# Kernel tuning notes

Measured on AMD Instinct MI355X. Metric: run time of the kernel, lower is better.

The kernel has to match this reference:

```python
import jax, jax.numpy as jnp
import numpy as np

KA = 2  # kernel_att == stride

def _unfold2(t):
    # torch nn.Unfold(kernel=2, stride=2, pad=0): [B,C,H,W] -> [B, C, 4, L], L=(H/2)*(W/2)
    B, C, H, W = t.shape
    t = t.reshape(B, C, H // KA, KA, W // KA, KA).transpose(0, 1, 3, 5, 2, 4)
    return t.reshape(B, C, KA * KA, (H // KA) * (W // KA))

def _fold2(t, H, W):
    # inverse of _unfold2 (non-overlapping): [B, C, 4, L] -> [B, C, H, W]
    B, C, _, L = t.shape
    t = t.reshape(B, C, KA, KA, H // KA, W // KA).transpose(0, 1, 4, 2, 5, 3)
    return t.reshape(B, C, H, W)

def setup_inputs() -> dict:
    key = jax.random.key(0)
    ks = jax.random.split(key, 5)
    b, c, m, h, w = 4, 16, 8, 64, 64
    O = 64
    return {
        "x": jax.random.normal(ks[0], (b, c, m, h, w), jnp.float32),
        "w_q": jax.random.normal(ks[1], (O, m), jnp.float32) * 0.1,
        "w_k": jax.random.normal(ks[2], (O, m), jnp.float32) * 0.1,
        "w_v": jax.random.normal(ks[3], (O, m), jnp.float32) * 0.1,
        "w_p": jax.random.normal(ks[4], (2,), jnp.float32) * 0.1,
    }

def reference(x, w_q, w_k, w_v, w_p):
    b, c, m, h, w = x.shape
    O = w_q.shape[0]
    # res = AdaptiveAvgPool3d((1, dim, dim)) with h==w==dim -> mean over m only
    res = x.mean(axis=2, keepdims=True)            # [b, c, 1, h, w]
    xf = x.reshape(b * c, m, h, w)
    # 1x1 convs (bias-free) are channel matmuls
    q = jnp.einsum('om,bmhw->bohw', w_q, xf)       # [b*c, O, h, w]
    k = jnp.einsum('om,bmhw->bohw', w_k, xf)
    v = jnp.einsum('om,bmhw->bohw', w_v, xf)
    # relative position map pe = conv_p(position(h, w)) -> [1,1,h,w]
    loc_w = jnp.linspace(-1.0, 1.0, w)[None, :]    # varies along W
    loc_h = jnp.linspace(-1.0, 1.0, h)[:, None]    # varies along H
    pe = (w_p[0] * loc_w + w_p[1] * loc_h)[None, None]  # [1,1,h,w]
    q5 = q.reshape(b, c, O, h, w).transpose(0, 2, 1, 3, 4)  # permuted: [b, O, c, h, w]
    k5 = k.reshape(b, c, O, h, w) + pe             # pe broadcast over trailing (h,w)
    v5 = v.reshape(b, c, O, h, w)
    scaling = float(h) ** (-0.5)
    B = b * O
    q_att = (q5 * scaling).reshape(B, c, h, w)
    # NB: torch code views the UNpermuted [b,c,O,h,w] buffer as [b*O, c, h, w] (raw reinterpretation)
    k_att = k5.reshape(B, c, h, w)
    v_att = v5.reshape(B, c, h, w)
    uq = _unfold2(q_att)                           # [B, c, 4, L]
    uk = _unfold2(k_att) + _unfold2(pe)            # unfold_rpe broadcast: [B, c, 4, L]
    uv = _unfold2(v_att)
    # att[B,i,j,l] = sum_p q[B,i,p,l] * k[B,j,p,l]
    att = jnp.einsum('bipl,bjpl->bijl', uq, uk)    # [B, c, c, L]
    att = jax.nn.softmax(att, axis=2)
    out = jnp.einsum('bijl,bjpl->bipl', att, uv)   # [B, c, 4, L]
    out = _fold2(out, h, w)                        # [B, c, h, w]
    out = out.reshape(b, O, c, h, w).transpose(0, 2, 1, 3, 4)  # [b, c, O, h, w]
    return out + res
```

## Files before the change

kernel.cpp:

```cpp
#include <hip/hip_runtime.h>

typedef float v2f __attribute__((ext_vector_type(2)));


__global__ __launch_bounds__(256, 4) void adapt_attn(
    const float* __restrict__ x,  const float* __restrict__ wq,
    const float* __restrict__ wk, const float* __restrict__ wv,
    const float* __restrict__ wp, float* __restrict__ out)
{
    __shared__ __align__(16) float s_wk[128];
    __shared__ __align__(16) float s_wv[128];
    __shared__ v2f    s_xk[2][8][2][16];
    __shared__ float4 s_uk[2][16][16];
    __shared__ float4 s_uv[2][16][16];

    const int tid = threadIdx.x;
    const int bid = blockIdx.x;
    const int tg = bid & 31;
    const int o  = (bid >> 5) & 63;
    const int bb = bid >> 11;
    const int r = o & 3, qch = o >> 2;

    const v2f* __restrict__ x2 = (const v2f*)x;

    v2f s1v[2];
    #pragma unroll
    for (int it = 0; it < 2; it++) {
        const int idx = it * 256 + tid;
        const int p = idx & 15, row = (idx >> 4) & 1, m = (idx >> 5) & 7, t = idx >> 8;
        const int tile = tg * 2 + t;
        const int y0 = (tile >> 1) << 1, ww0 = (tile & 1) << 4;
        s1v[it] = x2[((bb * 16 + qch) * 8 + m) * 2048 + (y0 + row) * 32 + ww0 + p];
    }

    float wkv_k = 0.f, wkv_v = 0.f;
    if (tid < 128) {
        wkv_k = wk[(r << 7) + tid];
        wkv_v = wv[(r << 7) + tid];
    }

    const int p3 = tid & 15, ig = (tid >> 4) & 7, t3 = tid >> 7;
    const int tile3 = tg * 2 + t3;
    const int y03 = (tile3 >> 1) << 1, ww03 = (tile3 & 1) << 4;
    const int sp = y03 * 32 + ww03 + p3;

    v2f qa0[8], qb0[8], qa1[8], qb1[8];
    {
        const int bq0 = (bb * 16 + ig * 2) * 16384 + sp;
        const int bq1 = bq0 + 16384;
        #pragma unroll
        for (int m = 0; m < 8; m++) {
            qa0[m] = x2[bq0 + m * 2048];
            qb0[m] = x2[bq0 + m * 2048 + 32];
            qa1[m] = x2[bq1 + m * 2048];
            qb1[m] = x2[bq1 + m * 2048 + 32];
        }
    }

    #pragma unroll
    for (int it = 0; it < 2; it++) {
        const int idx = it * 256 + tid;
        const int p = idx & 15, row = (idx >> 4) & 1, m = (idx >> 5) & 7, t = idx >> 8;
        s_xk[t][m][row][p] = s1v[it];
    }
    if (tid < 128) {
        s_wk[tid] = wkv_k;
        s_wv[tid] = wkv_v;
    }

    float wqr[8];
    #pragma unroll
    for (int m = 0; m < 8; m++) wqr[m] = 0.125f * wq[(o << 3) + m];

    v2f uqa0 = {0.f, 0.f}, uqb0 = {0.f, 0.f}, rsa0 = {0.f, 0.f}, rsb0 = {0.f, 0.f};
    v2f uqa1 = {0.f, 0.f}, uqb1 = {0.f, 0.f}, rsa1 = {0.f, 0.f}, rsb1 = {0.f, 0.f};
    #pragma unroll
    for (int m = 0; m < 8; m++) {
        uqa0 += qa0[m] * wqr[m];
        uqb0 += qb0[m] * wqr[m];
        rsa0 += qa0[m];
        rsb0 += qb0[m];
        uqa1 += qa1[m] * wqr[m];
        uqb1 += qb1[m] * wqr[m];
        rsa1 += qa1[m];
        rsb1 += qb1[m];
    }
    __syncthreads();

    const float wp0 = wp[0], wp1 = wp[1];
    const float step = 2.0f / 63.0f;
    #pragma unroll
    for (int it = 0; it < 2; it++) {
        const int idx = it * 256 + tid;
        const int p = idx & 15, j = (idx >> 4) & 15, t = idx >> 8;
        const int tile = tg * 2 + t;
        const int y0 = (tile >> 1) << 1, ww0 = (tile & 1) << 4;
        const int wwp = ww0 + p;
        const float lx0 = -1.0f + step * (float)(wwp << 1);
        const float lx1 = lx0 + step;
        const float ly0 = -1.0f + step * (float)y0;
        const float ly1 = ly0 + step;
        v2f ka = { 2.0f * (wp0 * lx0 + wp1 * ly0), 2.0f * (wp0 * lx1 + wp1 * ly0) };
        v2f kb = { 2.0f * (wp0 * lx0 + wp1 * ly1), 2.0f * (wp0 * lx1 + wp1 * ly1) };
        v2f va = {0.f, 0.f}, vb = {0.f, 0.f};

        float wkj[8], wvj[8];
        *(float4*)&wkj[0] = ((const float4*)s_wk)[j * 2];
        *(float4*)&wkj[4] = ((const float4*)s_wk)[j * 2 + 1];
        *(float4*)&wvj[0] = ((const float4*)s_wv)[j * 2];
        *(float4*)&wvj[4] = ((const float4*)s_wv)[j * 2 + 1];

        #pragma unroll
        for (int m = 0; m < 8; m++) {
            const v2f xa = s_xk[t][m][0][p];
            const v2f xb = s_xk[t][m][1][p];
            ka += xa * wkj[m]; kb += xb * wkj[m];
            va += xa * wvj[m]; vb += xb * wvj[m];
        }
        s_uk[t][j][p] = make_float4(ka.x, ka.y, kb.x, kb.y);
        s_uv[t][j][p] = make_float4(va.x, va.y, vb.x, vb.y);
    }
    __syncthreads();

    {
        v2f oa0 = {0.f, 0.f}, ob0 = {0.f, 0.f};
        v2f oa1 = {0.f, 0.f}, ob1 = {0.f, 0.f};
        float sum0 = 0.f, sum1 = 0.f;

        #pragma unroll
        for (int j = 0; j < 16; j++) {
            const float4 k4 = s_uk[t3][j][p3];
            const float4 v4 = s_uv[t3][j][p3];
            const v2f ka = {k4.x, k4.y}, kb = {k4.z, k4.w};
            const v2f va = {v4.x, v4.y}, vb = {v4.z, v4.w};

            v2f t0 = uqa0 * ka;
            t0 += uqb0 * kb;
            const float e0 = __expf(t0.x + t0.y);
            sum0 += e0;
            oa0 += va * e0;
            ob0 += vb * e0;

            v2f t1 = uqa1 * ka;
            t1 += uqb1 * kb;
            const float e1 = __expf(t1.x + t1.y);
            sum1 += e1;
            oa1 += va * e1;
            ob1 += vb * e1;
        }

        v2f* __restrict__ out2 = (v2f*)out;
        {
            const int i = ig * 2;
            const float rcp = 1.0f / sum0;
            const v2f outa = oa0 * rcp + rsa0 * 0.125f;
            const v2f outb = ob0 * rcp + rsb0 * 0.125f;
            const int obi = ((bb * 16 + i) * 64 + o) * 2048 + sp;
            out2[obi]      = outa;
            out2[obi + 32] = outb;
        }
        {
            const int i = ig * 2 + 1;
            const float rcp = 1.0f / sum1;
            const v2f outa = oa1 * rcp + rsa1 * 0.125f;
            const v2f outb = ob1 * rcp + rsb1 * 0.125f;
            const int obi = ((bb * 16 + i) * 64 + o) * 2048 + sp;
            out2[obi]      = outa;
            out2[obi + 32] = outb;
        }
    }
}

extern "C" void kernel_launch(void* const* d_in, const int* in_sizes, int n_in,
                              void* d_out, int out_size, void* d_ws, size_t ws_size,
                              hipStream_t stream) {
    const float* x  = (const float*)d_in[0];
    const float* wq = (const float*)d_in[1];
    const float* wk = (const float*)d_in[2];
    const float* wv = (const float*)d_in[3];
    const float* wp = (const float*)d_in[4];
    float* out = (float*)d_out;
    adapt_attn<<<dim3(8192), dim3(256), 0, stream>>>(x, wq, wk, wv, wp, out);
}
```

Measured before the change: 118.4 us.

## Double per-block tile work, 4 query rows per thread, native exp2

Each block now covers four 2x16 tiles instead of two, and the grid is halved. Every thread handles four query channels instead of two, so each K/V value read from shared memory feeds more softmax work. K/V weights are loaded straight from global memory into registers, which drops their shared-memory staging, and x is staged with float4 loads. Softmax now uses the hardware exp2 builtin with log2(e) folded into the query scale. The cost is higher register pressure and fewer blocks to spread across the GPU.

```diff
diff --git a/kernel.cpp b/kernel.cpp
--- a/kernel.cpp
+++ b/kernel.cpp
@@ -2,172 +2,157 @@
 
 typedef float v2f __attribute__((ext_vector_type(2)));
 
+
+#if __has_builtin(__builtin_amdgcn_exp2f)
+  #define EXP_FN(x) __builtin_amdgcn_exp2f(x)
+  #define QSCALE 0.18033688011112043f
+#else
+  #define EXP_FN(x) __expf(x)
+  #define QSCALE 0.125f
+#endif
 
 __global__ __launch_bounds__(256, 4) void adapt_attn(
     const float* __restrict__ x,  const float* __restrict__ wq,
     const float* __restrict__ wk, const float* __restrict__ wv,
     const float* __restrict__ wp, float* __restrict__ out)
 {
-    __shared__ __align__(16) float s_wk[128];
-    __shared__ __align__(16) float s_wv[128];
-    __shared__ v2f    s_xk[2][8][2][16];
-    __shared__ float4 s_uk[2][16][16];
-    __shared__ float4 s_uv[2][16][16];
+    __shared__ __align__(16) v2f s_xk[4][8][2][16];
+    __shared__ float4 s_uk[4][16][16];
+    __shared__ float4 s_uv[4][16][16];
 
     const int tid = threadIdx.x;
     const int bid = blockIdx.x;
-    const int tg = bid & 31;
-    const int o  = (bid >> 5) & 63;
-    const int bb = bid >> 11;
+    const int tq  = bid & 15;
+    const int o   = (bid >> 4) & 63;
+    const int bb  = bid >> 10;
     const int r = o & 3, qch = o >> 2;
 
-    const v2f* __restrict__ x2 = (const v2f*)x;
+    const v2f*    __restrict__ x2 = (const v2f*)x;
+    const float4* __restrict__ x4 = (const float4*)x;
 
-    v2f s1v[2];
+    float4 s1v[2];
     #pragma unroll
     for (int it = 0; it < 2; it++) {
         const int idx = it * 256 + tid;
-        const int p = idx & 15, row = (idx >> 4) & 1, m = (idx >> 5) & 7, t = idx >> 8;
-        const int tile = tg * 2 + t;
-        const int y0 = (tile >> 1) << 1, ww0 = (tile & 1) << 4;
-        s1v[it] = x2[((bb * 16 + qch) * 8 + m) * 2048 + (y0 + row) * 32 + ww0 + p];
+        const int f = idx & 7, row = (idx >> 3) & 1, m = (idx >> 4) & 7, t = idx >> 7;
+        const int y0 = tq * 4 + (t >> 1) * 2, w4 = (t & 1) * 8;
+        s1v[it] = x4[((bb * 16 + qch) * 8 + m) * 1024 + (y0 + row) * 16 + w4 + f];
     }
 
-    float wkv_k = 0.f, wkv_v = 0.f;
-    if (tid < 128) {
-        wkv_k = wk[(r << 7) + tid];
-        wkv_v = wv[(r << 7) + tid];
+    const int p3 = tid & 15, ig4 = (tid >> 4) & 3, t3 = tid >> 6;
+    const int y03 = tq * 4 + (t3 >> 1) * 2, ww03 = (t3 & 1) * 16;
+    const int sp = y03 * 32 + ww03 + p3;
+
+    float wqr[8];
+    #pragma unroll
+    for (int m = 0; m < 8; m++)
+        wqr[m] = QSCALE * wq[(o << 3) + m];
+
+    v2f uqa[4], uqb[4], rsa[4], rsb[4];
+    #pragma unroll
+    for (int ii = 0; ii < 4; ii++) {
+        const int i = ig4 * 4 + ii;
+        const int bq = (bb * 16 + i) * 16384 + sp;
+        v2f qa[8], qb[8];
+        #pragma unroll
+        for (int m = 0; m < 8; m++) {
+            qa[m] = x2[bq + m * 2048];
+            qb[m] = x2[bq + m * 2048 + 32];
+        }
+        v2f ua = {0.f,0.f}, ub = {0.f,0.f}, ra = {0.f,0.f}, rb = {0.f,0.f};
+        #pragma unroll
+        for (int m = 0; m < 8; m++) {
+            ua += qa[m] * wqr[m];  ub += qb[m] * wqr[m];
+            ra += qa[m];           rb += qb[m];
+        }
+        uqa[ii] = ua; uqb[ii] = ub; rsa[ii] = ra; rsb[ii] = rb;
     }
 
-    const int p3 = tid & 15, ig = (tid >> 4) & 7, t3 = tid >> 7;
-    const int tile3 = tg * 2 + t3;
-    const int y03 = (tile3 >> 1) << 1, ww03 = (tile3 & 1) << 4;
-    const int sp = y03 * 32 + ww03 + p3;
-
-    v2f qa0[8], qb0[8], qa1[8], qb1[8];
+    const int p2 = tid & 15, jg = (tid >> 4) & 7, th = tid >> 7;
+    const int j0 = jg * 2, j1 = j0 + 1;
+    float wk0[8], wk1[8], wv0[8], wv1[8];
     {
-        const int bq0 = (bb * 16 + ig * 2) * 16384 + sp;
-        const int bq1 = bq0 + 16384;
-        #pragma unroll
-        for (int m = 0; m < 8; m++) {
-            qa0[m] = x2[bq0 + m * 2048];
-            qb0[m] = x2[bq0 + m * 2048 + 32];
-            qa1[m] = x2[bq1 + m * 2048];
-            qb1[m] = x2[bq1 + m * 2048 + 32];
-        }
+        const float4* wk4 = (const float4*)wk;
+        const float4* wv4 = (const float4*)wv;
+        const int rb0 = (r * 16 + j0) * 2, rb1 = (r * 16 + j1) * 2;
+        *(float4*)&wk0[0] = wk4[rb0];     *(float4*)&wk0[4] = wk4[rb0 + 1];
+        *(float4*)&wk1[0] = wk4[rb1];     *(float4*)&wk1[4] = wk4[rb1 + 1];
+        *(float4*)&wv0[0] = wv4[rb0];     *(float4*)&wv0[4] = wv4[rb0 + 1];
+        *(float4*)&wv1[0] = wv4[rb1];     *(float4*)&wv1[4] = wv4[rb1 + 1];
     }
+    const float wp0 = wp[0], wp1 = wp[1];
 
     #pragma unroll
     for (int it = 0; it < 2; it++) {
         const int idx = it * 256 + tid;
-        const int p = idx & 15, row = (idx >> 4) & 1, m = (idx >> 5) & 7, t = idx >> 8;
-        s_xk[t][m][row][p] = s1v[it];
-    }
-    if (tid < 128) {
-        s_wk[tid] = wkv_k;
-        s_wv[tid] = wkv_v;
-    }
-
-    float wqr[8];
-    #pragma unroll
-    for (int m = 0; m < 8; m++) wqr[m] = 0.125f * wq[(o << 3) + m];
-
-    v2f uqa0 = {0.f, 0.f}, uqb0 = {0.f, 0.f}, rsa0 = {0.f, 0.f}, rsb0 = {0.f, 0.f};
-    v2f uqa1 = {0.f, 0.f}, uqb1 = {0.f, 0.f}, rsa1 = {0.f, 0.f}, rsb1 = {0.f, 0.f};
-    #pragma unroll
-    for (int m = 0; m < 8; m++) {
-        uqa0 += qa0[m] * wqr[m];
-        uqb0 += qb0[m] * wqr[m];
-        rsa0 += qa0[m];
-        rsb0 += qb0[m];
-        uqa1 += qa1[m] * wqr[m];
-        uqb1 += qb1[m] * wqr[m];
-        rsa1 += qa1[m];
-        rsb1 += qb1[m];
+        const int f = idx & 7, row = (idx >> 3) & 1, m = (idx >> 4) & 7, t = idx >> 7;
+        *(float4*)&s_xk[t][m][row][f * 2] = s1v[it];
     }
     __syncthreads();
 
-    const float wp0 = wp[0], wp1 = wp[1];
     const float step = 2.0f / 63.0f;
     #pragma unroll
-    for (int it = 0; it < 2; it++) {
-        const int idx = it * 256 + tid;
-        const int p = idx & 15, j = (idx >> 4) & 15, t = idx >> 8;
-        const int tile = tg * 2 + t;
-        const int y0 = (tile >> 1) << 1, ww0 = (tile & 1) << 4;
-        const int wwp = ww0 + p;
+    for (int tt2 = 0; tt2 < 2; tt2++) {
+        const int t = th * 2 + tt2;
+        const int y0 = tq * 4 + (t >> 1) * 2, ww0 = (t & 1) * 16;
+        const int wwp = ww0 + p2;
         const float lx0 = -1.0f + step * (float)(wwp << 1);
         const float lx1 = lx0 + step;
         const float ly0 = -1.0f + step * (float)y0;
         const float ly1 = ly0 + step;
-        v2f ka = { 2.0f * (wp0 * lx0 + wp1 * ly0), 2.0f * (wp0 * lx1 + wp1 * ly0) };
-        v2f kb = { 2.0f * (wp0 * lx0 + wp1 * ly1), 2.0f * (wp0 * lx1 + wp1 * ly1) };
-        v2f va = {0.f, 0.f}, vb = {0.f, 0.f};
-
-        float wkj[8], wvj[8];
-        *(float4*)&wkj[0] = ((const float4*)s_wk)[j * 2];
-        *(float4*)&wkj[4] = ((const float4*)s_wk)[j * 2 + 1];
-        *(float4*)&wvj[0] = ((const float4*)s_wv)[j * 2];
-        *(float4*)&wvj[4] = ((const float4*)s_wv)[j * 2 + 1];
-
+        const v2f pea = { 2.0f*(wp0*lx0 + wp1*ly0), 2.0f*(wp0*lx1 + wp1*ly0) };
+        const v2f peb = { 2.0f*(wp0*lx0 + wp1*ly1), 2.0f*(wp0*lx1 + wp1*ly1) };
+        v2f k0a = pea, k0b = peb, k1a = pea, k1b = peb;
+        v2f v0a = {0.f,0.f}, v0b = {0.f,0.f}, v1a = {0.f,0.f}, v1b = {0.f,0.f};
         #pragma unroll
         for (int m = 0; m < 8; m++) {
-            const v2f xa = s_xk[t][m][0][p];
-            const v2f xb = s_xk[t][m][1][p];
-            ka += xa * wkj[m]; kb += xb * wkj[m];
-            va += xa * wvj[m]; vb += xb * wvj[m];
+            const v2f xa = s_xk[t][m][0][p2];
+            const v2f xb = s_xk[t][m][1][p2];
+            k0a += xa * wk0[m];  k0b += xb * wk0[m];
+            k1a += xa * wk1[m];  k1b += xb * wk1[m];
+            v0a += xa * wv0[m];  v0b += xb * wv0[m];
+            v1a += xa * wv1[m];  v1b += xb * wv1[m];
         }
-        s_uk[t][j][p] = make_float4(ka.x, ka.y, kb.x, kb.y);
-        s_uv[t][j][p] = make_float4(va.x, va.y, vb.x, vb.y);
+        s_uk[t][j0][p2] = make_float4(k0a.x, k0a.y, k0b.x, k0b.y);
+        s_uk[t][j1][p2] = make_float4(k1a.x, k1a.y, k1b.x, k1b.y);
+        s_uv[t][j0][p2] = make_float4(v0a.x, v0a.y, v0b.x, v0b.y);
+        s_uv[t][j1][p2] = make_float4(v1a.x, v1a.y, v1b.x, v1b.y);
     }
     __syncthreads();
 
-    {
-        v2f oa0 = {0.f, 0.f}, ob0 = {0.f, 0.f};
-        v2f oa1 = {0.f, 0.f}, ob1 = {0.f, 0.f};
-        float sum0 = 0.f, sum1 = 0.f;
+    v2f oa[4], ob[4]; float sum[4];
+    #pragma unroll
+    for (int ii = 0; ii < 4; ii++) {
+        oa[ii] = (v2f){0.f,0.f}; ob[ii] = (v2f){0.f,0.f}; sum[ii] = 0.f;
+    }
 
+    #pragma unroll
+    for (int j = 0; j < 16; j++) {
+        const float4 k4 = s_uk[t3][j][p3];
+        const float4 v4 = s_uv[t3][j][p3];
+        const v2f ka = {k4.x, k4.y}, kb = {k4.z, k4.w};
+        const v2f va = {v4.x, v4.y}, vb = {v4.z, v4.w};
         #pragma unroll
-        for (int j = 0; j < 16; j++) {
-            const float4 k4 = s_uk[t3][j][p3];
-            const float4 v4 = s_uv[t3][j][p3];
-            const v2f ka = {k4.x, k4.y}, kb = {k4.z, k4.w};
-            const v2f va = {v4.x, v4.y}, vb = {v4.z, v4.w};
+        for (int ii = 0; ii < 4; ii++) {
+            v2f t0 = uqa[ii] * ka;
+            t0 += uqb[ii] * kb;
+            const float e = EXP_FN(t0.x + t0.y);
+            sum[ii] += e;
+            oa[ii] += va * e;
+            ob[ii] += vb * e;
+        }
+    }
 
-            v2f t0 = uqa0 * ka;
-            t0 += uqb0 * kb;
-            const float e0 = __expf(t0.x + t0.y);
-            sum0 += e0;
-            oa0 += va * e0;
-            ob0 += vb * e0;
-
-            v2f t1 = uqa1 * ka;
-            t1 += uqb1 * kb;
-            const float e1 = __expf(t1.x + t1.y);
-            sum1 += e1;
-            oa1 += va * e1;
-            ob1 += vb * e1;
-        }
-
-        v2f* __restrict__ out2 = (v2f*)out;
-        {
-            const int i = ig * 2;
-            const float rcp = 1.0f / sum0;
-            const v2f outa = oa0 * rcp + rsa0 * 0.125f;
-            const v2f outb = ob0 * rcp + rsb0 * 0.125f;
-            const int obi = ((bb * 16 + i) * 64 + o) * 2048 + sp;
-            out2[obi]      = outa;
-            out2[obi + 32] = outb;
-        }
-        {
-            const int i = ig * 2 + 1;
-            const float rcp = 1.0f / sum1;
-            const v2f outa = oa1 * rcp + rsa1 * 0.125f;
-            const v2f outb = ob1 * rcp + rsb1 * 0.125f;
-            const int obi = ((bb * 16 + i) * 64 + o) * 2048 + sp;
-            out2[obi]      = outa;
-            out2[obi + 32] = outb;
-        }
+    v2f* __restrict__ out2 = (v2f*)out;
+    #pragma unroll
+    for (int ii = 0; ii < 4; ii++) {
+        const int i = ig4 * 4 + ii;
+        const float rcp = 1.0f / sum[ii];
+        const v2f outa = oa[ii] * rcp + rsa[ii] * 0.125f;
+        const v2f outb = ob[ii] * rcp + rsb[ii] * 0.125f;
+        const int obi = ((bb * 16 + i) * 64 + o) * 2048 + sp;
+        out2[obi]      = outa;
+        out2[obi + 32] = outb;
     }
 }
 
@@ -180,5 +165,5 @@
     const float* wv = (const float*)d_in[3];
     const float* wp = (const float*)d_in[4];
     float* out = (float*)d_out;
-    adapt_attn<<<dim3(8192), dim3(256), 0, stream>>>(x, wq, wk, wv, wp, out);
+    adapt_attn<<<dim3(4096), dim3(256), 0, stream>>>(x, wq, wk, wv, wp, out);
 }
```

Result: slower. 120.8 us (+2.1%).
